# Performance work log

Measured on AMD Instinct MI355X. Metric: run time of the kernel, lower is better.

Reference implementation:

```python
import jax, jax.numpy as jnp
import numpy as np

N_NODES = 100000
N_EDGES = 600000
D = 128
HEADS = 8
REL = 9
N_GRAPHS = 64


def _relconv(h, coeff, basis, w_loop, b, src, dst, etypes, n_nodes):
    # DGL RelGraphConv, basis regularizer (num_bases == num_rels), sum aggregation,
    # self-loop, bias, relu activation (dropout inactive at eval).
    W = jnp.einsum('rb,bio->rio', coeff, basis)  # [REL, D, D]
    hsrc = h[src]                                # [E, D] gather
    msg = jnp.zeros((hsrc.shape[0], W.shape[2]), h.dtype)
    for r in range(REL):  # small fixed relation set
        msg = msg + jnp.where((etypes == r)[:, None], hsrc @ W[r], 0.0)
    agg = jax.ops.segment_sum(msg, dst, num_segments=n_nodes)
    return jax.nn.relu(agg + h @ w_loop + b)


def _graph_norm(x, seg, n_graphs, w, b, ms):
    # scatter-based per-subgraph normalization (graphNorm)
    counts = jax.ops.segment_sum(jnp.ones((x.shape[0],), x.dtype), seg, num_segments=n_graphs)[:, None]
    mean = jax.ops.segment_sum(x, seg, num_segments=n_graphs) / counts
    sub = x - mean[seg] * ms
    var = jax.ops.segment_sum(sub * sub, seg, num_segments=n_graphs) / counts
    std = jnp.sqrt(var + 1e-6)
    return w * sub / std[seg] + b


def _layer_norm(x, g, b):
    mu = x.mean(-1, keepdims=True)
    v = jnp.mean((x - mu) ** 2, -1, keepdims=True)
    return g * (x - mu) / jnp.sqrt(v + 1e-5) + b


def _forward(h, src, dst, etypes, seg, num_graphs,
             q_coeff, q_basis, q_loop, q_bias,
             k_coeff, k_basis, k_loop, k_bias,
             v_coeff, v_basis, v_loop, v_bias,
             o_w, o_b, gn1_w, gn1_b, gn1_ms, ln1_g, ln1_b,
             gn2_w, gn2_b, gn2_ms, ffn1_w, ffn1_b, ffn2_w, ffn2_b,
             ln2_g, ln2_b):
    n = h.shape[0]
    hn = _graph_norm(h, seg, num_graphs, gn1_w, gn1_b, gn1_ms)
    Q = _relconv(hn, q_coeff, q_basis, q_loop, q_bias, src, dst, etypes, n)
    K = _relconv(hn, k_coeff, k_basis, k_loop, k_bias, src, dst, etypes, n)
    V = _relconv(hn, v_coeff, v_basis, v_loop, v_bias, src, dst, etypes, n)
    dh = D // HEADS
    Qh = Q.reshape(n, HEADS, dh)
    Kh = K.reshape(n, HEADS, dh)
    Vh = V.reshape(n, HEADS, dh)
    # edge dot-product attention: score_e = <K[src], Q[dst]> per head
    score = (Kh[src] * Qh[dst]).sum(-1, keepdims=True)            # [E, H, 1]
    score = jnp.exp(jnp.clip(score / np.float32(np.sqrt(dh)), -10.0, 10.0))
    wV = jax.ops.segment_sum(Vh[src] * score, dst, num_segments=n)  # [N, H, dh]
    z = jax.ops.segment_sum(score, dst, num_segments=n)             # [N, H, 1]
    attn = (wV / (z + 1e-6)).reshape(n, D)
    hO = attn @ o_w + o_b
    h1 = _layer_norm(hO, ln1_g, ln1_b)
    h2 = _graph_norm(h1, seg, num_graphs, gn2_w, gn2_b, gn2_ms)
    h3 = jax.nn.relu(h2 @ ffn1_w + ffn1_b) @ ffn2_w + ffn2_b
    return _layer_norm(h3, ln2_g, ln2_b)


def setup_inputs() -> dict:
    key = jax.random.key(0)
    ks = jax.random.split(key, 32)
    s = np.float32(1.0 / np.sqrt(D))
    inp = {
        'h': jax.random.normal(ks[0], (N_NODES, D), jnp.float32),
        'src': jax.random.randint(ks[1], (N_EDGES,), 0, N_NODES),
        'dst': jax.random.randint(ks[2], (N_EDGES,), 0, N_NODES),
        'etypes': jax.random.randint(ks[3], (N_EDGES,), 0, REL),
        'seg': jnp.sort(jax.random.randint(ks[4], (N_NODES,), 0, N_GRAPHS)),
        'num_graphs': N_GRAPHS,
    }
    def lin(k, i, o):
        return jax.random.normal(k, (i, o), jnp.float32) / np.float32(np.sqrt(i))
    for idx, nm in enumerate(['q', 'k', 'v']):
        base = 5 + idx * 4
        inp[nm + '_coeff'] = jax.random.normal(ks[base], (REL, REL), jnp.float32) / np.float32(np.sqrt(REL))
        inp[nm + '_basis'] = jax.random.normal(ks[base + 1], (REL, D, D), jnp.float32) * s
        inp[nm + '_loop'] = lin(ks[base + 2], D, D)
        inp[nm + '_bias'] = jnp.zeros((D,), jnp.float32)
    inp['o_w'] = lin(ks[17], D, D)
    inp['o_b'] = jnp.zeros((D,), jnp.float32)
    for nm in ['gn1', 'gn2']:
        inp[nm + '_w'] = jnp.ones((D,), jnp.float32)
        inp[nm + '_b'] = jnp.zeros((D,), jnp.float32)
        inp[nm + '_ms'] = jnp.ones((D,), jnp.float32)
    inp['ln1_g'] = jnp.ones((D,), jnp.float32)
    inp['ln1_b'] = jnp.zeros((D,), jnp.float32)
    inp['ln2_g'] = jnp.ones((D,), jnp.float32)
    inp['ln2_b'] = jnp.zeros((D,), jnp.float32)
    inp['ffn1_w'] = lin(ks[18], D, 2 * D)
    inp['ffn1_b'] = jnp.zeros((2 * D,), jnp.float32)
    inp['ffn2_w'] = lin(ks[19], 2 * D, D)
    inp['ffn2_b'] = jnp.zeros((D,), jnp.float32)
    return inp


def reference(h, src, dst, etypes, seg, num_graphs,
              q_coeff, q_basis, q_loop, q_bias,
              k_coeff, k_basis, k_loop, k_bias,
              v_coeff, v_basis, v_loop, v_bias,
              o_w, o_b, gn1_w, gn1_b, gn1_ms, ln1_g, ln1_b,
              gn2_w, gn2_b, gn2_ms, ffn1_w, ffn1_b, ffn2_w, ffn2_b,
              ln2_g, ln2_b):
    return _forward(h, src, dst, etypes, seg, num_graphs,
                    q_coeff, q_basis, q_loop, q_bias,
                    k_coeff, k_basis, k_loop, k_bias,
                    v_coeff, v_basis, v_loop, v_bias,
                    o_w, o_b, gn1_w, gn1_b, gn1_ms, ln1_g, ln1_b,
                    gn2_w, gn2_b, gn2_ms, ffn1_w, ffn1_b, ffn2_w, ffn2_b,
                    ln2_g, ln2_b)
```

## Files before the change

kernel.cpp:

```cpp
#include <hip/hip_runtime.h>
#include <math.h>

#define N_NODES 100000
#define N_EDGES 600000
#define D 128
#define REL 9
#define NG 64
#define NK9 (N_NODES * REL)

typedef float f32x4 __attribute__((ext_vector_type(4)));
typedef _Float16 f16x8 __attribute__((ext_vector_type(8)));
typedef _Float16 h16x2 __attribute__((ext_vector_type(2)));

__device__ __forceinline__ ushort f2h(float x) {
    union { _Float16 h; ushort u; } c; c.h = (_Float16)x; return c.u;
}
__device__ __forceinline__ float h2f(ushort u) {
    union { ushort u; _Float16 h; } c; c.u = u; return (float)c.h;
}

__device__ __forceinline__ void ld16(const ushort* g, ushort* l) {
    __builtin_amdgcn_global_load_lds(
        (const __attribute__((address_space(1))) unsigned int*)g,
        (__attribute__((address_space(3))) unsigned int*)l, 16, 0, 0);
}

__device__ __forceinline__ int lbound(const int* __restrict__ a, int n, int key) {
    int lo = 0, hi = n;
    while (lo < hi) { int mid = (lo + hi) >> 1; if (a[mid] < key) lo = mid + 1; else hi = mid; }
    return lo;
}

__global__ void hist9_kernel(const int* __restrict__ dst, const int* __restrict__ ety,
                             int* __restrict__ cnt9) {
    int e = blockIdx.x * 256 + threadIdx.x;
    if (e < N_EDGES) atomicAdd(&cnt9[dst[e] * REL + ety[e]], 1);
}

__global__ void scan1_8(const int* __restrict__ cnt, int* __restrict__ excl,
                        int* __restrict__ bsum, int n) {
    __shared__ int s[1024];
    int tid = threadIdx.x;
    int base = blockIdx.x * 8192 + tid * 8;
    int v[8]; int sum = 0;
#pragma unroll
    for (int j = 0; j < 8; ++j) { v[j] = (base + j < n) ? cnt[base + j] : 0; sum += v[j]; }
    s[tid] = sum;
    __syncthreads();
    for (int off = 1; off < 1024; off <<= 1) {
        int t = (tid >= off) ? s[tid - off] : 0;
        __syncthreads();
        s[tid] += t;
        __syncthreads();
    }
    int run = s[tid] - sum;
#pragma unroll
    for (int j = 0; j < 8; ++j) { if (base + j < n) excl[base + j] = run; run += v[j]; }
    if (tid == 1023) bsum[blockIdx.x] = s[1023];
}

__global__ void scan2_kernel(int* __restrict__ bsum, int nb) {
    __shared__ int s[128];
    int tid = threadIdx.x;
    int v = (tid < nb) ? bsum[tid] : 0;
    s[tid] = v;
    __syncthreads();
    for (int off = 1; off < 128; off <<= 1) {
        int t = (tid >= off) ? s[tid - off] : 0;
        __syncthreads();
        s[tid] += t;
        __syncthreads();
    }
    if (tid < nb) bsum[tid] = s[tid] - v;
}

__global__ void scan3_8(int* __restrict__ excl, const int* __restrict__ bsum, int n, int total) {
    int base = blockIdx.x * 8192 + threadIdx.x * 8;
    int add = bsum[blockIdx.x];
#pragma unroll
    for (int j = 0; j < 8; ++j) if (base + j < n) excl[base + j] += add;
    if (blockIdx.x == 0 && threadIdx.x == 0) excl[n] = total;
}

__global__ void scatter9_kernel(const int* __restrict__ src, const int* __restrict__ dst,
                                const int* __restrict__ ety, const int* __restrict__ rstart,
                                int* __restrict__ cur9, int* __restrict__ ssrc) {
    int e = blockIdx.x * 256 + threadIdx.x;
    if (e < N_EDGES) {
        int key = dst[e] * REL + ety[e];
        int pos = rstart[key] + atomicAdd(&cur9[key], 1);
        ssrc[pos] = src[e];
    }
}

__global__ __launch_bounds__(256)
void gn_stats(const float* __restrict__ x, const int* __restrict__ seg,
              float* __restrict__ gsum, float* __restrict__ gsumsq) {
    int ch = threadIdx.x & 127;
    int rr = threadIdx.x >> 7;
    int n0 = blockIdx.x * 128;
    int nend = min(n0 + 128, N_NODES);
    float sx = 0.f, sxx = 0.f;
    int cg = -1;
    for (int n = n0 + rr; n < nend; n += 2) {
        int g = seg[n];
        if (g != cg) {
            if (cg >= 0) { atomicAdd(&gsum[cg * D + ch], sx); atomicAdd(&gsumsq[cg * D + ch], sxx); }
            cg = g; sx = 0.f; sxx = 0.f;
        }
        float v = x[(size_t)n * D + ch];
        sx += v; sxx += v * v;
    }
    if (cg >= 0) { atomicAdd(&gsum[cg * D + ch], sx); atomicAdd(&gsumsq[cg * D + ch], sxx); }
}

__global__ __launch_bounds__(256)
void gn_stats_h(const ushort* __restrict__ x, const int* __restrict__ seg,
                float* __restrict__ gsum, float* __restrict__ gsumsq) {
    int ch = threadIdx.x & 127;
    int rr = threadIdx.x >> 7;
    int n0 = blockIdx.x * 128;
    int nend = min(n0 + 128, N_NODES);
    float sx = 0.f, sxx = 0.f;
    int cg = -1;
    for (int n = n0 + rr; n < nend; n += 2) {
        int g = seg[n];
        if (g != cg) {
            if (cg >= 0) { atomicAdd(&gsum[cg * D + ch], sx); atomicAdd(&gsumsq[cg * D + ch], sxx); }
            cg = g; sx = 0.f; sxx = 0.f;
        }
        float v = h2f(x[(size_t)n * D + ch]);
        sx += v; sxx += v * v;
    }
    if (cg >= 0) { atomicAdd(&gsum[cg * D + ch], sx); atomicAdd(&gsumsq[cg * D + ch], sxx); }
}

__global__ void gn_final(const float* __restrict__ gsum, const float* __restrict__ gsumsq,
                         const int* __restrict__ seg, const float* __restrict__ w,
                         const float* __restrict__ b, const float* __restrict__ ms,
                         float* __restrict__ sc, float* __restrict__ off) {
    int g = blockIdx.x, ch = threadIdx.x;
    int lo = lbound(seg, N_NODES, g), hi = lbound(seg, N_NODES, g + 1);
    float cnt = (float)max(hi - lo, 1);
    float mean = gsum[g * D + ch] / cnt;
    float mm = mean * ms[ch];
    float var = gsumsq[g * D + ch] / cnt - 2.f * mm * mean + mm * mm;
    float rstd = rsqrtf(var + 1e-6f);
    float s = w[ch] * rstd;
    sc[g * D + ch] = s;
    off[g * D + ch] = b[ch] - s * mm;
}

__global__ __launch_bounds__(256)
void gn_apply(const float* __restrict__ x, const int* __restrict__ seg,
              const float* __restrict__ sc, const float* __restrict__ off,
              ushort* __restrict__ outhf) {
    int t = blockIdx.x * 256 + threadIdx.x;
    int n = t >> 6;
    if (n >= N_NODES) return;
    int ch = (t & 63) * 2;
    int g = seg[n];
    float2 xv = *(const float2*)&x[(size_t)n * D + ch];
    float2 s2 = *(const float2*)&sc[g * D + ch];
    float2 o2 = *(const float2*)&off[g * D + ch];
    ushort2 o;
    o.x = f2h(s2.x * xv.x + o2.x);
    o.y = f2h(s2.y * xv.y + o2.y);
    *(ushort2*)&outhf[(size_t)n * D + ch] = o;
}

__global__ __launch_bounds__(256)
void gn_apply_h(const ushort* __restrict__ x, const int* __restrict__ seg,
                const float* __restrict__ sc, const float* __restrict__ off,
                ushort* __restrict__ outhf) {
    int t = blockIdx.x * 256 + threadIdx.x;
    int n = t >> 6;
    if (n >= N_NODES) return;
    int ch = (t & 63) * 2;
    int g = seg[n];
    ushort2 xv = *(const ushort2*)&x[(size_t)n * D + ch];
    float2 s2 = *(const float2*)&sc[g * D + ch];
    float2 o2 = *(const float2*)&off[g * D + ch];
    ushort2 o;
    o.x = f2h(s2.x * h2f(xv.x) + o2.x);
    o.y = f2h(s2.y * h2f(xv.y) + o2.y);
    *(ushort2*)&outhf[(size_t)n * D + ch] = o;
}

__global__ void build_bt_qkv3(const float* __restrict__ c0, const float* __restrict__ c1,
                              const float* __restrict__ c2, const float* __restrict__ b0,
                              const float* __restrict__ b1, const float* __restrict__ b2,
                              const float* __restrict__ l0, const float* __restrict__ l1,
                              const float* __restrict__ l2, const float* __restrict__ i0,
                              const float* __restrict__ i1, const float* __restrict__ i2,
                              ushort* __restrict__ Btqkv, float* __restrict__ biasq) {
    int pj = blockIdx.y;
    const float* coeff  = pj == 0 ? c0 : (pj == 1 ? c1 : c2);
    const float* basis  = pj == 0 ? b0 : (pj == 1 ? b1 : b2);
    const float* loop_w = pj == 0 ? l0 : (pj == 1 ? l1 : l2);
    const float* bin    = pj == 0 ? i0 : (pj == 1 ? i1 : i2);
    ushort* Bt = Btqkv + (size_t)pj * 128 * 1280;
    int t = blockIdx.x * 256 + threadIdx.x;
    if (t < 128) biasq[pj * 128 + t] = bin[t];
    if (t >= 128 * 1280) return;
    int o = t / 1280;
    int k = t - o * 1280;
    float v;
    if (k < 128) {
        v = loop_w[k * 128 + o];
    } else {
        int kk = k - 128;
        int r = kk >> 7, i = kk & 127;
        v = 0.f;
#pragma unroll
        for (int b = 0; b < REL; ++b)
            v += coeff[r * REL + b] * basis[((size_t)b * 128 + i) * 128 + o];
    }
    Bt[(size_t)o * 1280 + k] = f2h(v);
}

__global__ void transpose_cast3(const float* __restrict__ o_w, ushort* __restrict__ Bto,
                                const float* __restrict__ f1, ushort* __restrict__ Btf1,
                                const float* __restrict__ f2, ushort* __restrict__ Btf2) {
    int t = blockIdx.x * 256 + threadIdx.x;
    if (t < 16384) {
        int n = t >> 7, k = t & 127;
        Bto[(size_t)n * 128 + k] = f2h(o_w[(size_t)k * 128 + n]);
    } else if (t < 49152) {
        int u = t - 16384;
        int n = u >> 7, k = u & 127;
        Btf1[(size_t)n * 128 + k] = f2h(f1[(size_t)k * 256 + n]);
    } else if (t < 81920) {
        int u = t - 49152;
        int n = u >> 8, k = u & 255;
        Btf2[(size_t)n * 256 + k] = f2h(f2[(size_t)k * 128 + n]);
    }
}

__global__ __launch_bounds__(512, 2)
void qkv_gemm_fused(const ushort* __restrict__ hnhf, const int* __restrict__ ssrc,
                    const int* __restrict__ rstart, const ushort* __restrict__ Bt,
                    const float* __restrict__ bias, ushort* __restrict__ Cout) {
    __shared__ ushort As[128 * 64];
    __shared__ ushort Bs[384 * 64];
    const int tid = threadIdx.x;
    const int lane = tid & 63;
    const int wave = tid >> 6;
    const int wm = wave & 1, wn = wave >> 1;
    const int quad = lane >> 4, l16 = lane & 15;
    const int row0 = blockIdx.x * 128;

    const ushort* sA[2];
#pragma unroll
    for (int i = 0; i < 2; ++i) {
        int rs = (wave * 2 + i) * 8 + (lane >> 3);
        int kg = (lane & 7) ^ (rs & 7);
        int ra = row0 + rs; if (ra >= N_NODES) ra = N_NODES - 1;
        sA[i] = hnhf + (size_t)ra * D + kg * 8;
    }
    const ushort* sB[6];
#pragma unroll
    for (int i = 0; i < 6; ++i) {
        int rs = (wave * 6 + i) * 8 + (lane >> 3);
        int kg = (lane & 7) ^ (rs & 7);
        sB[i] = Bt + (size_t)rs * 1280 + kg * 8;
    }

    const int grow = tid >> 2;
    const int sub = tid & 3;
    const int gnode = row0 + grow;
    const int gvalid = (gnode < N_NODES);
    const int gbase9 = gnode * REL;
    const int rw = grow & 7;

    f32x4 acc[4][6];
#pragma unroll
    for (int i = 0; i < 4; ++i)
#pragma unroll
        for (int j = 0; j < 6; ++j) acc[i][j] = (f32x4){0.f, 0.f, 0.f, 0.f};

    for (int kc = 0; kc < 1280; kc += 64) {
#pragma unroll
        for (int i = 0; i < 6; ++i) ld16(sB[i] + kc, &Bs[(wave * 6 + i) * 512]);
        if (kc < 128) {
#pragma unroll
            for (int i = 0; i < 2; ++i) ld16(sA[i] + kc, &As[(wave * 2 + i) * 512]);
        } else {
            int kk = kc - 128;
            int r = kk >> 7;
            int ch0 = kk & 64;
            f16x8 a0 = (f16x8)0, a1 = (f16x8)0;
            if (gvalid) {
                int e0 = rstart[gbase9 + r];
                int e1 = rstart[gbase9 + r + 1];
                for (int e = e0; e < e1; ++e) {
                    int s = ssrc[e];
                    const f16x8* hp = (const f16x8*)&hnhf[(size_t)s * D + ch0 + sub * 16];
                    a0 += hp[0];
                    a1 += hp[1];
                }
            }
            *(f16x8*)&As[grow * 64 + (((sub * 2) ^ rw) * 8)] = a0;
            *(f16x8*)&As[grow * 64 + (((sub * 2 + 1) ^ rw) * 8)] = a1;
        }
        __syncthreads();
#pragma unroll
        for (int h = 0; h < 2; ++h) {
            f16x8 af[4], bf[6];
#pragma unroll
            for (int i = 0; i < 4; ++i) {
                int rr = wm * 64 + i * 16 + l16;
                af[i] = *(const f16x8*)&As[rr * 64 + (((h * 4 + quad) ^ (rr & 7)) * 8)];
            }
#pragma unroll
            for (int j = 0; j < 6; ++j) {
                int cc = wn * 96 + j * 16 + l16;
                bf[j] = *(const f16x8*)&Bs[cc * 64 + (((h * 4 + quad) ^ (cc & 7)) * 8)];
            }
#pragma unroll
            for (int i = 0; i < 4; ++i)
#pragma unroll
                for (int j = 0; j < 6; ++j)
                    acc[i][j] = __builtin_amdgcn_mfma_f32_16x16x32_f16(af[i], bf[j], acc[i][j], 0, 0, 0);
        }
        __syncthreads();
    }

#pragma unroll
    for (int i = 0; i < 4; ++i) {
        int gr0 = row0 + wm * 64 + i * 16 + quad * 4;
#pragma unroll
        for (int r = 0; r < 4; ++r) {
            int gr = gr0 + r;
            if (gr >= N_NODES) continue;
#pragma unroll
            for (int j = 0; j < 6; ++j) {
                int gcol = wn * 96 + j * 16 + l16;
                float v = acc[i][j][r] + bias[gcol];
                v = fmaxf(v, 0.f);
                Cout[(size_t)gr * 384 + gcol] = f2h(v);
            }
        }
    }
}

template<bool SPLITA, bool RELU, bool F16OUT>
__global__ __launch_bounds__(256, 3)
void mfma_gemm(const ushort* __restrict__ A1, const ushort* __restrict__ A2, int lda2, int M,
               const ushort* __restrict__ Bt, int K,
               const float* __restrict__ bias, void* __restrict__ Cout, int ldc) {
    __shared__ ushort As[128 * 64];
    __shared__ ushort Bs[128 * 64];
    const int tid = threadIdx.x;
    const int lane = tid & 63;
    const int wave = tid >> 6;
    const int wm = wave & 1, wn = wave >> 1;
    const int quad = lane >> 4, l16 = lane & 15;
    const int col0 = blockIdx.x * 128, row0 = blockIdx.y * 128;

    const ushort* sA1[4];
    const ushort* sA2[4];
    const ushort* sB[4];
#pragma unroll
    for (int i = 0; i < 4; ++i) {
        int rs = (wave * 4 + i) * 8 + (lane >> 3);
        int kg = (lane & 7) ^ (rs & 7);
        int ra = row0 + rs; if (ra >= M) ra = M - 1;
        sA1[i] = SPLITA ? (A1 + (size_t)ra * 128 + kg * 8) : nullptr;
        sA2[i] = A2 + (size_t)ra * lda2 + kg * 8;
        sB[i]  = Bt + (size_t)(col0 + rs) * K + kg * 8;
    }

    f32x4 acc[4][4];
#pragma unroll
    for (int i = 0; i < 4; ++i)
#pragma unroll
        for (int j = 0; j < 4; ++j) acc[i][j] = (f32x4){0.f, 0.f, 0.f, 0.f};

    for (int kc = 0; kc < K; kc += 64) {
#pragma unroll
        for (int i = 0; i < 4; ++i) {
            const ushort* as = (SPLITA && kc < 128) ? (sA1[i] + kc) : (sA2[i] + (SPLITA ? kc - 128 : kc));
            ld16(as, &As[(wave * 4 + i) * 512]);
            ld16(sB[i] + kc, &Bs[(wave * 4 + i) * 512]);
        }
        __syncthreads();
#pragma unroll
        for (int h = 0; h < 2; ++h) {
            f16x8 af[4], bf[4];
#pragma unroll
            for (int i = 0; i < 4; ++i) {
                int r = wm * 64 + i * 16 + l16;
                af[i] = *(const f16x8*)&As[r * 64 + (((h * 4 + quad) ^ (r & 7)) * 8)];
                int c = wn * 64 + i * 16 + l16;
                bf[i] = *(const f16x8*)&Bs[c * 64 + (((h * 4 + quad) ^ (c & 7)) * 8)];
            }
#pragma unroll
            for (int i = 0; i < 4; ++i)
#pragma unroll
                for (int j = 0; j < 4; ++j)
                    acc[i][j] = __builtin_amdgcn_mfma_f32_16x16x32_f16(af[i], bf[j], acc[i][j], 0, 0, 0);
        }
        __syncthreads();
    }

#pragma unroll
    for (int i = 0; i < 4; ++i) {
        int gr0 = row0 + wm * 64 + i * 16 + quad * 4;
#pragma unroll
        for (int r = 0; r < 4; ++r) {
            int grow = gr0 + r;
            if (grow >= M) continue;
#pragma unroll
            for (int j = 0; j < 4; ++j) {
                int gcol = col0 + wn * 64 + j * 16 + l16;
                float v = acc[i][j][r] + bias[gcol];
                if (RELU) v = fmaxf(v, 0.f);
                if (F16OUT) ((ushort*)Cout)[(size_t)grow * ldc + gcol] = f2h(v);
                else        ((float*)Cout)[(size_t)grow * ldc + gcol] = v;
            }
        }
    }
}

template<bool F16OUT>
__global__ __launch_bounds__(256, 3)
void mfma_gemm_ln(const ushort* __restrict__ A, int lda, int M,
                  const ushort* __restrict__ Bt, int K,
                  const float* __restrict__ bias, const float* __restrict__ lng,
                  const float* __restrict__ lnb, void* __restrict__ Cout) {
    __shared__ ushort As[128 * 64];
    __shared__ ushort Bs[128 * 64];
    __shared__ float rsum[2][128];
    __shared__ float rsq[2][128];
    const int tid = threadIdx.x;
    const int lane = tid & 63;
    const int wave = tid >> 6;
    const int wm = wave & 1, wn = wave >> 1;
    const int quad = lane >> 4, l16 = lane & 15;
    const int row0 = blockIdx.y * 128;

    const ushort* sA[4];
    const ushort* sB[4];
#pragma unroll
    for (int i = 0; i < 4; ++i) {
        int rs = (wave * 4 + i) * 8 + (lane >> 3);
        int kg = (lane & 7) ^ (rs & 7);
        int ra = row0 + rs; if (ra >= M) ra = M - 1;
        sA[i] = A + (size_t)ra * lda + kg * 8;
        sB[i] = Bt + (size_t)rs * K + kg * 8;
    }

    f32x4 acc[4][4];
#pragma unroll
    for (int i = 0; i < 4; ++i)
#pragma unroll
        for (int j = 0; j < 4; ++j) acc[i][j] = (f32x4){0.f, 0.f, 0.f, 0.f};

    for (int kc = 0; kc < K; kc += 64) {
#pragma unroll
        for (int i = 0; i < 4; ++i) {
            ld16(sA[i] + kc, &As[(wave * 4 + i) * 512]);
            ld16(sB[i] + kc, &Bs[(wave * 4 + i) * 512]);
        }
        __syncthreads();
#pragma unroll
        for (int h = 0; h < 2; ++h) {
            f16x8 af[4], bf[4];
#pragma unroll
            for (int i = 0; i < 4; ++i) {
                int r = wm * 64 + i * 16 + l16;
                af[i] = *(const f16x8*)&As[r * 64 + (((h * 4 + quad) ^ (r & 7)) * 8)];
                int c = wn * 64 + i * 16 + l16;
                bf[i] = *(const f16x8*)&Bs[c * 64 + (((h * 4 + quad) ^ (c & 7)) * 8)];
            }
#pragma unroll
            for (int i = 0; i < 4; ++i)
#pragma unroll
                for (int j = 0; j < 4; ++j)
                    acc[i][j] = __builtin_amdgcn_mfma_f32_16x16x32_f16(af[i], bf[j], acc[i][j], 0, 0, 0);
        }
        __syncthreads();
    }

#pragma unroll
    for (int i = 0; i < 4; ++i) {
#pragma unroll
        for (int r = 0; r < 4; ++r) {
            float s = 0.f, q = 0.f;
#pragma unroll
            for (int j = 0; j < 4; ++j) {
                float v = acc[i][j][r] + bias[wn * 64 + j * 16 + l16];
                s += v; q += v * v;
            }
            s += __shfl_xor(s, 1); q += __shfl_xor(q, 1);
            s += __shfl_xor(s, 2); q += __shfl_xor(q, 2);
            s += __shfl_xor(s, 4); q += __shfl_xor(q, 4);
            s += __shfl_xor(s, 8); q += __shfl_xor(q, 8);
            if (l16 == 0) {
                int row = wm * 64 + i * 16 + quad * 4 + r;
                rsum[wn][row] = s;
                rsq[wn][row] = q;
            }
        }
    }
    __syncthreads();

#pragma unroll
    for (int i = 0; i < 4; ++i) {
#pragma unroll
        for (int r = 0; r < 4; ++r) {
            int row = wm * 64 + i * 16 + quad * 4 + r;
            int grow = row0 + row;
            if (grow >= M) continue;
            float tot = rsum[0][row] + rsum[1][row];
            float tq  = rsq[0][row] + rsq[1][row];
            float mu = tot * (1.f / 128.f);
            float var = tq * (1.f / 128.f) - mu * mu;
            float rstd = rsqrtf(var + 1e-5f);
#pragma unroll
            for (int j = 0; j < 4; ++j) {
                int gcol = wn * 64 + j * 16 + l16;
                float v = acc[i][j][r] + bias[gcol];
                float o = lng[gcol] * (v - mu) * rstd + lnb[gcol];
                if (F16OUT) ((ushort*)Cout)[(size_t)grow * 128 + gcol] = f2h(o);
                else        ((float*)Cout)[(size_t)grow * 128 + gcol] = o;
            }
        }
    }
}

__global__ __launch_bounds__(256)
void attn_kernel(const ushort* __restrict__ C, const int* __restrict__ ssrc,
                 const int* __restrict__ rstart, ushort* __restrict__ attnhf) {
    int n = (blockIdx.x * 256 + threadIdx.x) >> 6;
    if (n >= N_NODES) return;
    int lane = threadIdx.x & 63;
    h16x2 qh = *(const h16x2*)&C[(size_t)n * 384 + 2 * lane];
    int e0 = rstart[n * REL], e1 = rstart[n * REL + REL];
    float wvx = 0.f, wvy = 0.f, z = 0.f;
    int e = e0;
    for (; e + 2 <= e1; e += 2) {
        int s0 = ssrc[e], s1 = ssrc[e + 1];
        h16x2 k0 = *(const h16x2*)&C[(size_t)s0 * 384 + 128 + 2 * lane];
        h16x2 k1 = *(const h16x2*)&C[(size_t)s1 * 384 + 128 + 2 * lane];
        h16x2 v0 = *(const h16x2*)&C[(size_t)s0 * 384 + 256 + 2 * lane];
        h16x2 v1 = *(const h16x2*)&C[(size_t)s1 * 384 + 256 + 2 * lane];
        float d0 = __builtin_amdgcn_fdot2(k0, qh, 0.f, false);
        float d1 = __builtin_amdgcn_fdot2(k1, qh, 0.f, false);
        d0 += __shfl_xor(d0, 1); d1 += __shfl_xor(d1, 1);
        d0 += __shfl_xor(d0, 2); d1 += __shfl_xor(d1, 2);
        d0 += __shfl_xor(d0, 4); d1 += __shfl_xor(d1, 4);
        float sc0 = __expf(fminf(fmaxf(d0 * 0.25f, -10.f), 10.f));
        float sc1 = __expf(fminf(fmaxf(d1 * 0.25f, -10.f), 10.f));
        wvx += sc0 * (float)v0.x + sc1 * (float)v1.x;
        wvy += sc0 * (float)v0.y + sc1 * (float)v1.y;
        z += sc0 + sc1;
    }
    if (e < e1) {
        int s0 = ssrc[e];
        h16x2 k0 = *(const h16x2*)&C[(size_t)s0 * 384 + 128 + 2 * lane];
        h16x2 v0 = *(const h16x2*)&C[(size_t)s0 * 384 + 256 + 2 * lane];
        float d0 = __builtin_amdgcn_fdot2(k0, qh, 0.f, false);
        d0 += __shfl_xor(d0, 1);
        d0 += __shfl_xor(d0, 2);
        d0 += __shfl_xor(d0, 4);
        float sc0 = __expf(fminf(fmaxf(d0 * 0.25f, -10.f), 10.f));
        wvx += sc0 * (float)v0.x;
        wvy += sc0 * (float)v0.y;
        z += sc0;
    }
    float inv = 1.f / (z + 1e-6f);
    ushort2 o;
    o.x = f2h(wvx * inv);
    o.y = f2h(wvy * inv);
    *(ushort2*)&attnhf[(size_t)n * D + 2 * lane] = o;
}

extern "C" void kernel_launch(void* const* d_in, const int* in_sizes, int n_in,
                              void* d_out, int out_size, void* d_ws, size_t ws_size,
                              hipStream_t stream) {
    (void)in_sizes; (void)n_in; (void)out_size; (void)ws_size;
    const float* h     = (const float*)d_in[0];
    const int*   src   = (const int*)d_in[1];
    const int*   dst   = (const int*)d_in[2];
    const int*   ety   = (const int*)d_in[3];
    const int*   seg   = (const int*)d_in[4];
    const float* coeffs[3] = {(const float*)d_in[6],  (const float*)d_in[10], (const float*)d_in[14]};
    const float* bases [3] = {(const float*)d_in[7],  (const float*)d_in[11], (const float*)d_in[15]};
    const float* loops [3] = {(const float*)d_in[8],  (const float*)d_in[12], (const float*)d_in[16]};
    const float* pbias [3] = {(const float*)d_in[9],  (const float*)d_in[13], (const float*)d_in[17]};
    const float* o_w   = (const float*)d_in[18];
    const float* o_b   = (const float*)d_in[19];
    const float* gn1_w = (const float*)d_in[20];
    const float* gn1_b = (const float*)d_in[21];
    const float* gn1_ms= (const float*)d_in[22];
    const float* gn2_w = (const float*)d_in[23];
    const float* gn2_b = (const float*)d_in[24];
    const float* gn2_ms= (const float*)d_in[25];
    const float* ln1_g = (const float*)d_in[26];
    const float* ln1_b = (const float*)d_in[27];
    const float* ln2_g = (const float*)d_in[28];
    const float* ln2_b = (const float*)d_in[29];
    const float* ffn1_w= (const float*)d_in[30];
    const float* ffn1_b= (const float*)d_in[31];
    const float* ffn2_w= (const float*)d_in[32];
    const float* ffn2_b= (const float*)d_in[33];

    char* p = (char*)d_ws;
    auto take = [&](size_t bytes) { char* r = p; p += (bytes + 255) & ~(size_t)255; return r; };
    int*    cnt9   = (int*)take((size_t)NK9 * 2 * 4);
    int*    cur9   = cnt9 + NK9;
    int*    rstart = (int*)take((size_t)(NK9 + 8) * 4);
    int*    bsum   = (int*)take(512);
    int*    ssrc   = (int*)take((size_t)N_EDGES * 4);
    float*  gsum   = (float*)take((size_t)NG * D * 4 * 2);
    float*  gsumsq = gsum + NG * D;
    float*  gsc    = (float*)take((size_t)NG * D * 4);
    float*  goff   = (float*)take((size_t)NG * D * 4);
    ushort* Btqkv  = (ushort*)take((size_t)384 * 1280 * 2);
    float*  biasq  = (float*)take(384 * 4);
    ushort* Bto    = (ushort*)take((size_t)128 * 128 * 2);
    ushort* Btf1   = (ushort*)take((size_t)256 * 128 * 2);
    ushort* Btf2   = (ushort*)take((size_t)128 * 256 * 2);
    ushort* hnhf   = (ushort*)take((size_t)N_NODES * D * 2);
    ushort* attnhf = (ushort*)take((size_t)N_NODES * D * 2);
    ushort* h1hf   = (ushort*)take((size_t)N_NODES * D * 2);
    ushort* Cqkv   = (ushort*)take((size_t)N_NODES * 384 * 2);

    ushort* gn2hf  = Cqkv;
    ushort* ffn1hf = (ushort*)((char*)Cqkv + 25600000);

    const int EB = (N_EDGES + 255) / 256;
    const int KB = (NK9 + 8191) / 8192;
    const int WB = (N_NODES * 64 + 255) / 256;
    const int GB = (N_NODES + 127) / 128;
    const int RB = (N_NODES + 127) / 128;

    hipMemsetAsync(cnt9, 0, (size_t)NK9 * 8, stream);
    hist9_kernel<<<EB, 256, 0, stream>>>(dst, ety, cnt9);
    scan1_8<<<KB, 1024, 0, stream>>>(cnt9, rstart, bsum, NK9);
    scan2_kernel<<<1, 128, 0, stream>>>(bsum, KB);
    scan3_8<<<KB, 1024, 0, stream>>>(rstart, bsum, NK9, N_EDGES);
    scatter9_kernel<<<EB, 256, 0, stream>>>(src, dst, ety, rstart, cur9, ssrc);

    build_bt_qkv3<<<dim3(640, 3), 256, 0, stream>>>(
        coeffs[0], coeffs[1], coeffs[2], bases[0], bases[1], bases[2],
        loops[0], loops[1], loops[2], pbias[0], pbias[1], pbias[2], Btqkv, biasq);
    transpose_cast3<<<320, 256, 0, stream>>>(o_w, Bto, ffn1_w, Btf1, ffn2_w, Btf2);

    hipMemsetAsync(gsum, 0, (size_t)NG * D * 8, stream);
    gn_stats<<<GB, 256, 0, stream>>>(h, seg, gsum, gsumsq);
    gn_final<<<NG, 128, 0, stream>>>(gsum, gsumsq, seg, gn1_w, gn1_b, gn1_ms, gsc, goff);
    gn_apply<<<WB, 256, 0, stream>>>(h, seg, gsc, goff, hnhf);

    qkv_gemm_fused<<<RB, 512, 0, stream>>>(hnhf, ssrc, rstart, Btqkv, biasq, Cqkv);

    attn_kernel<<<WB, 256, 0, stream>>>(Cqkv, ssrc, rstart, attnhf);

    mfma_gemm_ln<true><<<dim3(1, RB), 256, 0, stream>>>(
        attnhf, 128, N_NODES, Bto, 128, o_b, ln1_g, ln1_b, h1hf);

    hipMemsetAsync(gsum, 0, (size_t)NG * D * 8, stream);
    gn_stats_h<<<GB, 256, 0, stream>>>(h1hf, seg, gsum, gsumsq);
    gn_final<<<NG, 128, 0, stream>>>(gsum, gsumsq, seg, gn2_w, gn2_b, gn2_ms, gsc, goff);
    gn_apply_h<<<WB, 256, 0, stream>>>(h1hf, seg, gsc, goff, gn2hf);

    mfma_gemm<false, true, true><<<dim3(2, RB), 256, 0, stream>>>(
        nullptr, gn2hf, 128, N_NODES, Btf1, 128, ffn1_b, ffn1hf, 256);
    mfma_gemm_ln<false><<<dim3(1, RB), 256, 0, stream>>>(
        ffn1hf, 256, N_NODES, Btf2, 256, ffn2_b, ln2_g, ln2_b, (float*)d_out);
}
```

Measured before the change: 790.5 us.

## Gather all relation aggregates into LDS first, then stream weights from global

Rewrites the fused QKV kernel so each block handles 64 nodes. It first gathers the self row and all nine per-relation neighbour sums into a 160KB dynamic LDS tile in one pass over the node's sorted edge list, with four source loads in flight at a time. The MFMA loop then reads A fragments from LDS and takes B fragments straight from global/L2 with register double-buffering. This removes the 20 per-chunk barriers and the repeated per-relation rstart walks. In exchange it uses very large LDS, so occupancy drops to one block per CU, and weight traffic through L2 rises.

```diff
diff --git a/kernel.cpp b/kernel.cpp
--- a/kernel.cpp
+++ b/kernel.cpp
@@ -237,98 +237,140 @@
     }
 }
 
-__global__ __launch_bounds__(512, 2)
-void qkv_gemm_fused(const ushort* __restrict__ hnhf, const int* __restrict__ ssrc,
-                    const int* __restrict__ rstart, const ushort* __restrict__ Bt,
-                    const float* __restrict__ bias, ushort* __restrict__ Cout) {
-    __shared__ ushort As[128 * 64];
-    __shared__ ushort Bs[384 * 64];
+__global__ __launch_bounds__(512)
+void qkv_v2(const ushort* __restrict__ hnhf, const int* __restrict__ ssrc,
+            const int* __restrict__ rstart, const ushort* __restrict__ Bt,
+            const float* __restrict__ bias, ushort* __restrict__ Cout) {
+    extern __shared__ ushort Sp[];
     const int tid = threadIdx.x;
+    const int row0 = blockIdx.x * 64;
+
+    {
+        const int prow = tid >> 3;
+        const int ps = tid & 7;
+        const int node = row0 + prow;
+        const int nclamp = node < N_NODES ? node : N_NODES - 1;
+        const int rw = prow & 7;
+        const int rbase = prow * 1280;
+        const int kg0 = (2 * ps) & 7;
+        const int tloop = ps >> 2;
+        const int slot0 = (kg0 ^ rw) * 8;
+        const int slot1 = ((kg0 + 1) ^ rw) * 8;
+
+        int rs1 = 0, rs2 = 0, rs3 = 0, rs4 = 0, rs5 = 0, rs6 = 0, rs7 = 0, rs8 = 0;
+        int e = 0, eend = 0;
+        if (node < N_NODES) {
+            const int* rp = rstart + node * REL;
+            e = rp[0];
+            rs1 = rp[1]; rs2 = rp[2]; rs3 = rp[3]; rs4 = rp[4];
+            rs5 = rp[5]; rs6 = rp[6]; rs7 = rp[7]; rs8 = rp[8];
+            eend = rp[9];
+        }
+
+        const ushort* lp = &hnhf[(size_t)nclamp * 128 + ps * 16];
+        f16x8 l0 = *(const f16x8*)lp;
+        f16x8 l1 = *(const f16x8*)(lp + 8);
+        *(f16x8*)&Sp[rbase + tloop * 64 + slot0] = l0;
+        *(f16x8*)&Sp[rbase + tloop * 64 + slot1] = l1;
+
+        f16x8 a0 = (f16x8)0, a1 = (f16x8)0;
+        int cur = 0;
+#define RELOF(ee) (((ee) >= rs1) + ((ee) >= rs2) + ((ee) >= rs3) + ((ee) >= rs4) + \
+                   ((ee) >= rs5) + ((ee) >= rs6) + ((ee) >= rs7) + ((ee) >= rs8))
+#define FLUSH(rk) while (cur < (rk)) { int tb = (2 + 2 * cur + tloop) * 64; \
+            *(f16x8*)&Sp[rbase + tb + slot0] = a0; \
+            *(f16x8*)&Sp[rbase + tb + slot1] = a1; \
+            a0 = (f16x8)0; a1 = (f16x8)0; ++cur; }
+        while (e < eend) {
+            int ec = eend - 1;
+            int i0 = ssrc[e];
+            int i1 = ssrc[e + 1 < eend ? e + 1 : ec];
+            int i2 = ssrc[e + 2 < eend ? e + 2 : ec];
+            int i3 = ssrc[e + 3 < eend ? e + 3 : ec];
+            const ushort* p0 = &hnhf[(size_t)i0 * 128 + ps * 16];
+            const ushort* p1 = &hnhf[(size_t)i1 * 128 + ps * 16];
+            const ushort* p2 = &hnhf[(size_t)i2 * 128 + ps * 16];
+            const ushort* p3 = &hnhf[(size_t)i3 * 128 + ps * 16];
+            f16x8 v0a = *(const f16x8*)p0, v0b = *(const f16x8*)(p0 + 8);
+            f16x8 v1a = *(const f16x8*)p1, v1b = *(const f16x8*)(p1 + 8);
+            f16x8 v2a = *(const f16x8*)p2, v2b = *(const f16x8*)(p2 + 8);
+            f16x8 v3a = *(const f16x8*)p3, v3b = *(const f16x8*)(p3 + 8);
+            { int rk = RELOF(e); FLUSH(rk) a0 += v0a; a1 += v0b; }
+            if (e + 1 < eend) { int rk = RELOF(e + 1); FLUSH(rk) a0 += v1a; a1 += v1b; }
+            if (e + 2 < eend) { int rk = RELOF(e + 2); FLUSH(rk) a0 += v2a; a1 += v2b; }
+            if (e + 3 < eend) { int rk = RELOF(e + 3); FLUSH(rk) a0 += v3a; a1 += v3b; }
+            e += 4;
+        }
+        FLUSH(9)
+#undef FLUSH
+#undef RELOF
+    }
+    __syncthreads();
+
     const int lane = tid & 63;
     const int wave = tid >> 6;
     const int wm = wave & 1, wn = wave >> 1;
     const int quad = lane >> 4, l16 = lane & 15;
-    const int row0 = blockIdx.x * 128;
-
-    const ushort* sA[2];
+
+    const ushort* bp[6];
+#pragma unroll
+    for (int j = 0; j < 6; ++j)
+        bp[j] = Bt + (size_t)(wn * 96 + j * 16 + l16) * 1280 + quad * 8;
+
+    int arow[2], aslt0[2], aslt1[2];
 #pragma unroll
     for (int i = 0; i < 2; ++i) {
-        int rs = (wave * 2 + i) * 8 + (lane >> 3);
-        int kg = (lane & 7) ^ (rs & 7);
-        int ra = row0 + rs; if (ra >= N_NODES) ra = N_NODES - 1;
-        sA[i] = hnhf + (size_t)ra * D + kg * 8;
-    }
-    const ushort* sB[6];
-#pragma unroll
-    for (int i = 0; i < 6; ++i) {
-        int rs = (wave * 6 + i) * 8 + (lane >> 3);
-        int kg = (lane & 7) ^ (rs & 7);
-        sB[i] = Bt + (size_t)rs * 1280 + kg * 8;
-    }
-
-    const int grow = tid >> 2;
-    const int sub = tid & 3;
-    const int gnode = row0 + grow;
-    const int gvalid = (gnode < N_NODES);
-    const int gbase9 = gnode * REL;
-    const int rw = grow & 7;
-
-    f32x4 acc[4][6];
-#pragma unroll
-    for (int i = 0; i < 4; ++i)
+        int r = wm * 32 + i * 16 + l16;
+        arow[i] = r * 1280;
+        aslt0[i] = (quad ^ (r & 7)) * 8;
+        aslt1[i] = ((4 + quad) ^ (r & 7)) * 8;
+    }
+
+    f32x4 acc[2][6];
+#pragma unroll
+    for (int i = 0; i < 2; ++i)
 #pragma unroll
         for (int j = 0; j < 6; ++j) acc[i][j] = (f32x4){0.f, 0.f, 0.f, 0.f};
 
-    for (int kc = 0; kc < 1280; kc += 64) {
-#pragma unroll
-        for (int i = 0; i < 6; ++i) ld16(sB[i] + kc, &Bs[(wave * 6 + i) * 512]);
-        if (kc < 128) {
-#pragma unroll
-            for (int i = 0; i < 2; ++i) ld16(sA[i] + kc, &As[(wave * 2 + i) * 512]);
-        } else {
-            int kk = kc - 128;
-            int r = kk >> 7;
-            int ch0 = kk & 64;
-            f16x8 a0 = (f16x8)0, a1 = (f16x8)0;
-            if (gvalid) {
-                int e0 = rstart[gbase9 + r];
-                int e1 = rstart[gbase9 + r + 1];
-                for (int e = e0; e < e1; ++e) {
-                    int s = ssrc[e];
-                    const f16x8* hp = (const f16x8*)&hnhf[(size_t)s * D + ch0 + sub * 16];
-                    a0 += hp[0];
-                    a1 += hp[1];
-                }
-            }
-            *(f16x8*)&As[grow * 64 + (((sub * 2) ^ rw) * 8)] = a0;
-            *(f16x8*)&As[grow * 64 + (((sub * 2 + 1) ^ rw) * 8)] = a1;
-        }
-        __syncthreads();
-#pragma unroll
-        for (int h = 0; h < 2; ++h) {
-            f16x8 af[4], bf[6];
-#pragma unroll
-            for (int i = 0; i < 4; ++i) {
-                int rr = wm * 64 + i * 16 + l16;
-                af[i] = *(const f16x8*)&As[rr * 64 + (((h * 4 + quad) ^ (rr & 7)) * 8)];
-            }
-#pragma unroll
-            for (int j = 0; j < 6; ++j) {
-                int cc = wn * 96 + j * 16 + l16;
-                bf[j] = *(const f16x8*)&Bs[cc * 64 + (((h * 4 + quad) ^ (cc & 7)) * 8)];
-            }
-#pragma unroll
-            for (int i = 0; i < 4; ++i)
-#pragma unroll
-                for (int j = 0; j < 6; ++j)
-                    acc[i][j] = __builtin_amdgcn_mfma_f32_16x16x32_f16(af[i], bf[j], acc[i][j], 0, 0, 0);
-        }
-        __syncthreads();
-    }
-
-#pragma unroll
-    for (int i = 0; i < 4; ++i) {
-        int gr0 = row0 + wm * 64 + i * 16 + quad * 4;
+    f16x8 bf0[6], bf1[6];
+#pragma unroll
+    for (int j = 0; j < 6; ++j) {
+        bf0[j] = *(const f16x8*)(bp[j]);
+        bf1[j] = *(const f16x8*)(bp[j] + 32);
+    }
+
+    for (int t = 0; t < 20; ++t) {
+        const int kc = t * 64;
+        const int kn = (t < 19) ? kc + 64 : kc;
+        f16x8 bn0[6], bn1[6];
+#pragma unroll
+        for (int j = 0; j < 6; ++j) {
+            bn0[j] = *(const f16x8*)(bp[j] + kn);
+            bn1[j] = *(const f16x8*)(bp[j] + kn + 32);
+        }
+        f16x8 af0[2], af1[2];
+#pragma unroll
+        for (int i = 0; i < 2; ++i) {
+            af0[i] = *(const f16x8*)&Sp[arow[i] + kc + aslt0[i]];
+            af1[i] = *(const f16x8*)&Sp[arow[i] + kc + aslt1[i]];
+        }
+#pragma unroll
+        for (int i = 0; i < 2; ++i)
+#pragma unroll
+            for (int j = 0; j < 6; ++j)
+                acc[i][j] = __builtin_amdgcn_mfma_f32_16x16x32_f16(af0[i], bf0[j], acc[i][j], 0, 0, 0);
+#pragma unroll
+        for (int i = 0; i < 2; ++i)
+#pragma unroll
+            for (int j = 0; j < 6; ++j)
+                acc[i][j] = __builtin_amdgcn_mfma_f32_16x16x32_f16(af1[i], bf1[j], acc[i][j], 0, 0, 0);
+#pragma unroll
+        for (int j = 0; j < 6; ++j) { bf0[j] = bn0[j]; bf1[j] = bn1[j]; }
+    }
+
+#pragma unroll
+    for (int i = 0; i < 2; ++i) {
+        int gr0 = row0 + wm * 32 + i * 16 + quad * 4;
 #pragma unroll
         for (int r = 0; r < 4; ++r) {
             int gr = gr0 + r;
@@ -636,6 +678,7 @@
     const int WB = (N_NODES * 64 + 255) / 256;
     const int GB = (N_NODES + 127) / 128;
     const int RB = (N_NODES + 127) / 128;
+    const int QB = (N_NODES + 63) / 64;
 
     hipMemsetAsync(cnt9, 0, (size_t)NK9 * 8, stream);
     hist9_kernel<<<EB, 256, 0, stream>>>(dst, ety, cnt9);
@@ -654,7 +697,8 @@
     gn_final<<<NG, 128, 0, stream>>>(gsum, gsumsq, seg, gn1_w, gn1_b, gn1_ms, gsc, goff);
     gn_apply<<<WB, 256, 0, stream>>>(h, seg, gsc, goff, hnhf);
 
-    qkv_gemm_fused<<<RB, 512, 0, stream>>>(hnhf, ssrc, rstart, Btqkv, biasq, Cqkv);
+    hipFuncSetAttribute((const void*)qkv_v2, hipFuncAttributeMaxDynamicSharedMemorySize, 163840);
+    qkv_v2<<<QB, 512, 163840, stream>>>(hnhf, ssrc, rstart, Btqkv, biasq, Cqkv);
 
     attn_kernel<<<WB, 256, 0, stream>>>(Cqkv, ssrc, rstart, attnhf);
 
```

Measured after the change: 974.3 us. 23.3% more time.

## Split relation-aggregation out of QKV GEMM into a separate per-node pass

Applied to the files above, without the earlier changes.

Replaces the fused gather-inside-GEMM with a separate s_pass kernel that, per destination node, walks all incoming edges once and accumulates neighbour features into 9 per-relation fp16 buffers, written to a workspace matrix. The GEMM then loads A tiles with async global-to-LDS copies instead of doing irregular gathers between barriers. The scatter now also stores each edge's type so the aggregation can pick the relation bucket with a wave-uniform switch. This trades the gather stalls inside the GEMM for an extra write and read of a large N×1152 fp16 intermediate, processed in chunks when the workspace is small.

```diff
diff --git a/kernel.cpp b/kernel.cpp
--- a/kernel.cpp
+++ b/kernel.cpp
@@ -84,12 +84,15 @@
 
 __global__ void scatter9_kernel(const int* __restrict__ src, const int* __restrict__ dst,
                                 const int* __restrict__ ety, const int* __restrict__ rstart,
-                                int* __restrict__ cur9, int* __restrict__ ssrc) {
+                                int* __restrict__ cur9, int* __restrict__ ssrc,
+                                int* __restrict__ setp) {
     int e = blockIdx.x * 256 + threadIdx.x;
     if (e < N_EDGES) {
-        int key = dst[e] * REL + ety[e];
+        int t = ety[e];
+        int key = dst[e] * REL + t;
         int pos = rstart[key] + atomicAdd(&cur9[key], 1);
         ssrc[pos] = src[e];
+        setp[pos] = t;
     }
 }
 
@@ -237,10 +240,47 @@
     }
 }
 
-__global__ __launch_bounds__(512, 2)
-void qkv_gemm_fused(const ushort* __restrict__ hnhf, const int* __restrict__ ssrc,
-                    const int* __restrict__ rstart, const ushort* __restrict__ Bt,
-                    const float* __restrict__ bias, ushort* __restrict__ Cout) {
+__global__ __launch_bounds__(256)
+void s_pass(const ushort* __restrict__ hnhf, const int* __restrict__ ssrc,
+            const int* __restrict__ setp, const int* __restrict__ rstart,
+            ushort* __restrict__ Ab, int c0, int c1) {
+    int n = c0 + ((blockIdx.x * 256 + threadIdx.x) >> 6);
+    if (n >= c1) return;
+    int lane = threadIdx.x & 63;
+    int e0 = rstart[n * REL], e1 = rstart[n * REL + REL];
+    h16x2 a0 = (h16x2)0, a1 = (h16x2)0, a2 = (h16x2)0, a3 = (h16x2)0, a4 = (h16x2)0;
+    h16x2 a5 = (h16x2)0, a6 = (h16x2)0, a7 = (h16x2)0, a8 = (h16x2)0;
+#define ACC(rr, hv) switch (rr) { \
+        case 0: a0 += hv; break; case 1: a1 += hv; break; case 2: a2 += hv; break; \
+        case 3: a3 += hv; break; case 4: a4 += hv; break; case 5: a5 += hv; break; \
+        case 6: a6 += hv; break; case 7: a7 += hv; break; default: a8 += hv; break; }
+    int e = e0;
+    for (; e + 2 <= e1; e += 2) {
+        int s0 = ssrc[e], s1 = ssrc[e + 1];
+        int r0 = __builtin_amdgcn_readfirstlane(setp[e]);
+        int r1 = __builtin_amdgcn_readfirstlane(setp[e + 1]);
+        h16x2 hv0 = *(const h16x2*)&hnhf[(size_t)s0 * D + 2 * lane];
+        h16x2 hv1 = *(const h16x2*)&hnhf[(size_t)s1 * D + 2 * lane];
+        ACC(r0, hv0)
+        ACC(r1, hv1)
+    }
+    if (e < e1) {
+        int s0 = ssrc[e];
+        int r0 = __builtin_amdgcn_readfirstlane(setp[e]);
+        h16x2 hv0 = *(const h16x2*)&hnhf[(size_t)s0 * D + 2 * lane];
+        ACC(r0, hv0)
+    }
+#undef ACC
+    ushort* arow = Ab + (size_t)(n - c0) * 1152;
+#define ST(r) *(h16x2*)&arow[r * 128 + 2 * lane] = a##r;
+    ST(0) ST(1) ST(2) ST(3) ST(4) ST(5) ST(6) ST(7) ST(8)
+#undef ST
+}
+
+__global__ __launch_bounds__(512)
+void mfma_gemm384(const ushort* __restrict__ A1, const ushort* __restrict__ Ab, int M,
+                  const ushort* __restrict__ Bt, const float* __restrict__ bias,
+                  ushort* __restrict__ Cout) {
     __shared__ ushort As[128 * 64];
     __shared__ ushort Bs[384 * 64];
     const int tid = threadIdx.x;
@@ -250,13 +290,15 @@
     const int quad = lane >> 4, l16 = lane & 15;
     const int row0 = blockIdx.x * 128;
 
-    const ushort* sA[2];
+    const ushort* sA1[2];
+    const ushort* sA2[2];
 #pragma unroll
     for (int i = 0; i < 2; ++i) {
         int rs = (wave * 2 + i) * 8 + (lane >> 3);
         int kg = (lane & 7) ^ (rs & 7);
-        int ra = row0 + rs; if (ra >= N_NODES) ra = N_NODES - 1;
-        sA[i] = hnhf + (size_t)ra * D + kg * 8;
+        int ra = row0 + rs; if (ra >= M) ra = M - 1;
+        sA1[i] = A1 + (size_t)ra * 128 + kg * 8;
+        sA2[i] = Ab + (size_t)ra * 1152 + kg * 8;
     }
     const ushort* sB[6];
 #pragma unroll
@@ -266,13 +308,6 @@
         sB[i] = Bt + (size_t)rs * 1280 + kg * 8;
     }
 
-    const int grow = tid >> 2;
-    const int sub = tid & 3;
-    const int gnode = row0 + grow;
-    const int gvalid = (gnode < N_NODES);
-    const int gbase9 = gnode * REL;
-    const int rw = grow & 7;
-
     f32x4 acc[4][6];
 #pragma unroll
     for (int i = 0; i < 4; ++i)
@@ -282,26 +317,10 @@
     for (int kc = 0; kc < 1280; kc += 64) {
 #pragma unroll
         for (int i = 0; i < 6; ++i) ld16(sB[i] + kc, &Bs[(wave * 6 + i) * 512]);
-        if (kc < 128) {
-#pragma unroll
-            for (int i = 0; i < 2; ++i) ld16(sA[i] + kc, &As[(wave * 2 + i) * 512]);
-        } else {
-            int kk = kc - 128;
-            int r = kk >> 7;
-            int ch0 = kk & 64;
-            f16x8 a0 = (f16x8)0, a1 = (f16x8)0;
-            if (gvalid) {
-                int e0 = rstart[gbase9 + r];
-                int e1 = rstart[gbase9 + r + 1];
-                for (int e = e0; e < e1; ++e) {
-                    int s = ssrc[e];
-                    const f16x8* hp = (const f16x8*)&hnhf[(size_t)s * D + ch0 + sub * 16];
-                    a0 += hp[0];
-                    a1 += hp[1];
-                }
-            }
-            *(f16x8*)&As[grow * 64 + (((sub * 2) ^ rw) * 8)] = a0;
-            *(f16x8*)&As[grow * 64 + (((sub * 2 + 1) ^ rw) * 8)] = a1;
+#pragma unroll
+        for (int i = 0; i < 2; ++i) {
+            const ushort* as = (kc < 128) ? (sA1[i] + kc) : (sA2[i] + (kc - 128));
+            ld16(as, &As[(wave * 2 + i) * 512]);
         }
         __syncthreads();
 #pragma unroll
@@ -309,13 +328,13 @@
             f16x8 af[4], bf[6];
 #pragma unroll
             for (int i = 0; i < 4; ++i) {
-                int rr = wm * 64 + i * 16 + l16;
-                af[i] = *(const f16x8*)&As[rr * 64 + (((h * 4 + quad) ^ (rr & 7)) * 8)];
+                int r = wm * 64 + i * 16 + l16;
+                af[i] = *(const f16x8*)&As[r * 64 + (((h * 4 + quad) ^ (r & 7)) * 8)];
             }
 #pragma unroll
             for (int j = 0; j < 6; ++j) {
-                int cc = wn * 96 + j * 16 + l16;
-                bf[j] = *(const f16x8*)&Bs[cc * 64 + (((h * 4 + quad) ^ (cc & 7)) * 8)];
+                int c = wn * 96 + j * 16 + l16;
+                bf[j] = *(const f16x8*)&Bs[c * 64 + (((h * 4 + quad) ^ (c & 7)) * 8)];
             }
 #pragma unroll
             for (int i = 0; i < 4; ++i)
@@ -328,11 +347,11 @@
 
 #pragma unroll
     for (int i = 0; i < 4; ++i) {
-        int gr0 = row0 + wm * 64 + i * 16 + quad * 4;
+        int gr0 = wm * 64 + i * 16 + quad * 4 + row0;
 #pragma unroll
         for (int r = 0; r < 4; ++r) {
             int gr = gr0 + r;
-            if (gr >= N_NODES) continue;
+            if (gr >= M) continue;
 #pragma unroll
             for (int j = 0; j < 6; ++j) {
                 int gcol = wn * 96 + j * 16 + l16;
@@ -580,7 +599,7 @@
 extern "C" void kernel_launch(void* const* d_in, const int* in_sizes, int n_in,
                               void* d_out, int out_size, void* d_ws, size_t ws_size,
                               hipStream_t stream) {
-    (void)in_sizes; (void)n_in; (void)out_size; (void)ws_size;
+    (void)in_sizes; (void)n_in; (void)out_size;
     const float* h     = (const float*)d_in[0];
     const int*   src   = (const int*)d_in[1];
     const int*   dst   = (const int*)d_in[2];
@@ -614,6 +633,7 @@
     int*    rstart = (int*)take((size_t)(NK9 + 8) * 4);
     int*    bsum   = (int*)take(512);
     int*    ssrc   = (int*)take((size_t)N_EDGES * 4);
+    int*    setp   = (int*)take((size_t)N_EDGES * 4);
     float*  gsum   = (float*)take((size_t)NG * D * 4 * 2);
     float*  gsumsq = gsum + NG * D;
     float*  gsc    = (float*)take((size_t)NG * D * 4);
@@ -627,6 +647,13 @@
     ushort* attnhf = (ushort*)take((size_t)N_NODES * D * 2);
     ushort* h1hf   = (ushort*)take((size_t)N_NODES * D * 2);
     ushort* Cqkv   = (ushort*)take((size_t)N_NODES * 384 * 2);
+    size_t used = (size_t)(p - (char*)d_ws);
+    size_t avail = (ws_size > used) ? ws_size - used : 0;
+    int NC = 1;
+    if (avail < (size_t)N_NODES * 1152 * 2) NC = 4;
+    if (NC == 4 && avail < ((size_t)(N_NODES / 4 + 1) * 1152 * 2)) NC = 8;
+    ushort* Ab = (ushort*)p;
+    const int chunk = (N_NODES + NC - 1) / NC;
 
     ushort* gn2hf  = Cqkv;
     ushort* ffn1hf = (ushort*)((char*)Cqkv + 25600000);
@@ -642,7 +669,7 @@
     scan1_8<<<KB, 1024, 0, stream>>>(cnt9, rstart, bsum, NK9);
     scan2_kernel<<<1, 128, 0, stream>>>(bsum, KB);
     scan3_8<<<KB, 1024, 0, stream>>>(rstart, bsum, NK9, N_EDGES);
-    scatter9_kernel<<<EB, 256, 0, stream>>>(src, dst, ety, rstart, cur9, ssrc);
+    scatter9_kernel<<<EB, 256, 0, stream>>>(src, dst, ety, rstart, cur9, ssrc, setp);
 
     build_bt_qkv3<<<dim3(640, 3), 256, 0, stream>>>(
         coeffs[0], coeffs[1], coeffs[2], bases[0], bases[1], bases[2],
@@ -654,7 +681,15 @@
     gn_final<<<NG, 128, 0, stream>>>(gsum, gsumsq, seg, gn1_w, gn1_b, gn1_ms, gsc, goff);
     gn_apply<<<WB, 256, 0, stream>>>(h, seg, gsc, goff, hnhf);
 
-    qkv_gemm_fused<<<RB, 512, 0, stream>>>(hnhf, ssrc, rstart, Btqkv, biasq, Cqkv);
+    for (int c = 0; c < NC; ++c) {
+        int c0 = c * chunk;
+        int c1 = min(N_NODES, c0 + chunk);
+        int rows = c1 - c0;
+        if (rows <= 0) break;
+        s_pass<<<(rows + 3) / 4, 256, 0, stream>>>(hnhf, ssrc, setp, rstart, Ab, c0, c1);
+        mfma_gemm384<<<(rows + 127) / 128, 512, 0, stream>>>(
+            hnhf + (size_t)c0 * 128, Ab, rows, Btqkv, biasq, Cqkv + (size_t)c0 * 384);
+    }
 
     attn_kernel<<<WB, 256, 0, stream>>>(Cqkv, ssrc, rstart, attnhf);
 
```

After: 790.7 us. About the same (+0.0%).
